# Kernel tuning notes

Measured on AMD Instinct MI355X. Metric: run time of the kernel, lower is better.

The kernel has to match this reference:

```python
import jax, jax.numpy as jnp
import numpy as np
import math

N, M = 512, 31
INP, EMB, ATT = 64, 64, 64
NUM_RELS = 200
SELF_LOOP_IDX = NUM_RELS  # index num_rels is the self-loop relation


def setup_inputs() -> dict:
    key = jax.random.key(0)
    ks = jax.random.split(key, 11)
    s_w = 1.0 / math.sqrt(EMB)
    return {
        "h": jax.random.normal(ks[0], (N, INP), jnp.float32),
        "msg": jax.random.normal(ks[1], (N, M, EMB), jnp.float32),
        "msg_type": jax.random.randint(ks[2], (N, M), 0, NUM_RELS, jnp.int32),
        "r_label_node": jax.random.randint(ks[3], (N,), 0, NUM_RELS, jnp.int32),
        "r_label_msg": jax.random.randint(ks[4], (N, M), 0, NUM_RELS, jnp.int32),
        "W_self": jax.random.normal(ks[5], (INP, EMB), jnp.float32) * s_w,
        "Q": jax.random.normal(ks[6], (NUM_RELS + 1, EMB, ATT), jnp.float32) * s_w,
        "K": jax.random.normal(ks[7], (NUM_RELS + 1, EMB, ATT), jnp.float32) * s_w,
        "V": jax.random.normal(ks[8], (NUM_RELS + 1, EMB, ATT), jnp.float32) * s_w,
        "ffn_w": jax.random.normal(ks[9], (ATT, EMB), jnp.float32) * s_w,
        "ffn_b": jnp.zeros((EMB,), jnp.float32),
    }


def reference(h, msg, msg_type, r_label_node, r_label_msg, W_self, Q, K, V, ffn_w, ffn_b):
    curr = h @ W_self                                        # [N, EMB]
    x = jnp.concatenate([curr[:, None, :], msg], axis=1)     # [N, M+1, EMB]
    qv_idx = jnp.concatenate([r_label_node[:, None], r_label_msg], axis=1)  # [N, M+1]
    self_col = jnp.full((x.shape[0], 1), SELF_LOOP_IDX, msg_type.dtype)
    k_idx = jnp.concatenate([self_col, msg_type], axis=1)    # [N, M+1]
    # relation-indexed per-token projection weights (irregular gather)
    q = jnp.einsum("nme,nmea->nma", x, Q[qv_idx])            # [N, M+1, ATT]
    k = jnp.einsum("nme,nmea->nma", x, K[k_idx])             # [N, M+1, ATT]
    v = jnp.einsum("nme,nmea->nma", x, V[qv_idx])            # [N, M+1, ATT]
    scores = jnp.einsum("nqa,nka->nqk", q, k) / math.sqrt(ATT)
    # NOTE: original code applies softmax over dim=1 (the query axis)
    att = jax.nn.softmax(scores, axis=1)                     # [N, M+1, M+1]
    pooled = jnp.einsum("nqk,nka->nqa", att, v)[:, 0]        # [N, ATT]
    return pooled @ ffn_w + ffn_b                            # [N, EMB]
```

## Files before the change

### kernel.cpp

```cpp
#include <hip/hip_runtime.h>
#include <math.h>

#define NN 512
#define MM 31
#define TT 32
#define EE 64
#define NREL 200
#define NMAT 201
#define SELF_LOOP 200
#define QCAP 192
#define NT 6
#define WSTR 72
#define CPAD 32

typedef short  short8 __attribute__((ext_vector_type(8)));
typedef float  f32x4  __attribute__((ext_vector_type(4)));

__device__ __forceinline__ unsigned short f2bf(float f) {
    union { float f; unsigned int u; } a; a.f = f;
    unsigned int r = a.u + 0x7FFFu + ((a.u >> 16) & 1u);
    return (unsigned short)(r >> 16);
}
__device__ __forceinline__ float bf2f(unsigned short u) {
    union { unsigned int u; float f; } a; a.u = ((unsigned int)u) << 16;
    return a.f;
}

__global__ __launch_bounds__(256) void prep_convert_kernel(
    const float* __restrict__ h, const float* __restrict__ W_self,
    const float* __restrict__ Q, const float* __restrict__ K,
    const float* __restrict__ V,
    const int* __restrict__ msg_type, const int* __restrict__ r_label_node,
    const int* __restrict__ r_label_msg, const float* __restrict__ msg,
    int* __restrict__ cnt_q, int* __restrict__ cnt_k,
    int* __restrict__ list_q, int* __restrict__ list_k,
    unsigned short* __restrict__ wt_q, unsigned short* __restrict__ wt_k,
    unsigned short* __restrict__ wt_v,
    unsigned short* __restrict__ msg_bf, unsigned short* __restrict__ curr_bf,
    unsigned short* __restrict__ k_bf)
{
    const int bid = blockIdx.x, tid = threadIdx.x;

    if (bid < 3 * NMAT) {
        const int r   = bid % NMAT;
        const int mat = bid / NMAT;
        const float* src = (mat == 0 ? Q : mat == 1 ? K : V) + (size_t)r * EE * EE;
        unsigned short* dst = (mat == 0 ? wt_q : mat == 1 ? wt_k : wt_v)
                              + (size_t)r * EE * EE;
        __shared__ unsigned short t_s[EE * WSTR];
        {
            const int e = tid >> 2, aseg = (tid & 3) * 16;
            const float4* s4 = (const float4*)(src + e * EE + aseg);
            float4 f0 = s4[0], f1 = s4[1], f2 = s4[2], f3 = s4[3];
            unsigned short b[16] = {
                f2bf(f0.x), f2bf(f0.y), f2bf(f0.z), f2bf(f0.w),
                f2bf(f1.x), f2bf(f1.y), f2bf(f1.z), f2bf(f1.w),
                f2bf(f2.x), f2bf(f2.y), f2bf(f2.z), f2bf(f2.w),
                f2bf(f3.x), f2bf(f3.y), f2bf(f3.z), f2bf(f3.w) };
            unsigned short* d = &t_s[e * WSTR + aseg];
            *(short8*)d = *(short8*)&b[0];
            *(short8*)(d + 8) = *(short8*)&b[8];
        }
        __syncthreads();
        {
            const int a = tid >> 2, eseg = (tid & 3) * 16;
            unsigned short o[16];
#pragma unroll
            for (int j = 0; j < 16; ++j)
                o[j] = t_s[(eseg + j) * WSTR + a];
            unsigned short* d = dst + a * EE + eseg;
            *(short8*)d = *(short8*)&o[0];
            *(short8*)(d + 8) = *(short8*)&o[8];
        }
        return;
    }

    const int n = bid - 3 * NMAT;

    if (tid < MM) {
        int j  = n * MM + tid;
        int rl = r_label_msg[j];
        int p  = atomicAdd(&cnt_q[rl * CPAD], 1);
        if (p < QCAP) list_q[rl * QCAP + p] = n * TT + tid + 1;
        int mt = msg_type[j];
        int p2 = atomicAdd(&cnt_k[mt * CPAD], 1);
        if (p2 < QCAP) list_k[mt * QCAP + p2] = n * TT + tid + 1;
    } else if (tid == 63) {
        int r = r_label_node[n];
        int p = atomicAdd(&cnt_q[r * CPAD], 1);
        if (p < QCAP) list_q[r * QCAP + p] = n * TT;
    }

    if (tid < MM * EE / 8) {
        const float4* s4 = (const float4*)(msg + (size_t)n * MM * EE) + tid * 2;
        float4 f0 = s4[0], f1 = s4[1];
        unsigned short b[8] = { f2bf(f0.x), f2bf(f0.y), f2bf(f0.z), f2bf(f0.w),
                                f2bf(f1.x), f2bf(f1.y), f2bf(f1.z), f2bf(f1.w) };
        *(short8*)(msg_bf + (size_t)n * MM * EE + tid * 8) = *(short8*)b;
    }

    __shared__ float c_s[EE];
    if (tid < EE) {
        const float* hrow = h + n * EE;
        float acc = 0.f;
#pragma unroll 8
        for (int e = 0; e < EE; ++e)
            acc = fmaf(hrow[e], W_self[e * EE + tid], acc);
        curr_bf[n * EE + tid] = f2bf(acc);
        c_s[tid] = acc;
    }
    __syncthreads();
    if (tid < EE) {
        const float* K200 = K + (size_t)SELF_LOOP * EE * EE;
        float k0 = 0.f;
#pragma unroll 8
        for (int e = 0; e < EE; ++e)
            k0 = fmaf(c_s[e], K200[e * EE + tid], k0);
        k_bf[(size_t)n * TT * EE + tid] = f2bf(k0);
    }
}

__global__ __launch_bounds__(256) void proj_tile_kernel(
    const unsigned short* __restrict__ curr_bf,
    const unsigned short* __restrict__ msg_bf,
    const unsigned short* __restrict__ wt_q,
    const unsigned short* __restrict__ wt_k,
    const unsigned short* __restrict__ wt_v,
    const int* __restrict__ cnt_q, const int* __restrict__ cnt_k,
    const int* __restrict__ list_q, const int* __restrict__ list_k,
    unsigned short* __restrict__ q_bf, unsigned short* __restrict__ k_bf,
    unsigned short* __restrict__ v_bf)
{
    const int r    = blockIdx.x / NT;
    const int tile = blockIdx.x % NT;
    const int tid  = threadIdx.x;
    const int lane = tid & 63;
    const int wave = tid >> 6;
    const int col  = lane & 15;
    const int quad = lane >> 4;

    const int nq = min(cnt_q[r * CPAD], QCAP);
    const int nk = min(cnt_k[r * CPAD], QCAP);
    const int q0 = tile * 32;
    const bool do_q = q0 < nq;
    const bool do_k = q0 < nk;
    if (!do_q && !do_k) return;

    const size_t wbase = (size_t)r * EE * EE;

    if (do_q) {
        const int mtile = wave & 1;
        const unsigned short* wmat = ((wave >> 1) ? wt_v : wt_q) + wbase;
        unsigned short* outp = (wave >> 1) ? v_bf : q_bf;
        const int arow = q0 + mtile * 16 + col;
        int atok = (arow < nq) ? list_q[r * QCAP + arow] : 0;
        {
            int an = atok >> 5, at = atok & 31;
            const unsigned short* aptr = at
                ? (msg_bf + ((size_t)an * MM + (at - 1)) * EE)
                : (curr_bf + (size_t)an * EE);
            f32x4 acc[4] = {{0,0,0,0},{0,0,0,0},{0,0,0,0},{0,0,0,0}};
#pragma unroll
            for (int kk = 0; kk < 2; ++kk) {
                short8 af = *(const short8*)(aptr + kk * 32 + quad * 8);
#pragma unroll
                for (int nt = 0; nt < 4; ++nt) {
                    short8 bf = *(const short8*)(wmat + (nt * 16 + col) * EE + kk * 32 + quad * 8);
                    acc[nt] = __builtin_amdgcn_mfma_f32_16x16x32_bf16(af, bf, acc[nt], 0, 0, 0);
                }
            }
#pragma unroll
            for (int reg = 0; reg < 4; ++reg) {
                int rrow = q0 + mtile * 16 + quad * 4 + reg;
                if (rrow < nq) {
                    int token = list_q[r * QCAP + rrow];
#pragma unroll
                    for (int nt = 0; nt < 4; ++nt)
                        outp[(size_t)token * EE + nt * 16 + col] = f2bf(acc[nt][reg]);
                }
            }
        }
    }

    if (do_k) {
        const int mtile = wave & 1;
        const int nh = wave >> 1;
        const int arow = q0 + mtile * 16 + col;
        int atok = (arow < nk) ? list_k[r * QCAP + arow] : 0;
        int an = atok >> 5, at = atok & 31;
        const unsigned short* aptr = at
            ? (msg_bf + ((size_t)an * MM + (at - 1)) * EE)
            : (curr_bf + (size_t)an * EE);
        const unsigned short* wmat = wt_k + wbase;
        f32x4 acc[2] = {{0,0,0,0},{0,0,0,0}};
#pragma unroll
        for (int kk = 0; kk < 2; ++kk) {
            short8 af = *(const short8*)(aptr + kk * 32 + quad * 8);
#pragma unroll
            for (int j = 0; j < 2; ++j) {
                int nt = nh * 2 + j;
                short8 bf = *(const short8*)(wmat + (nt * 16 + col) * EE + kk * 32 + quad * 8);
                acc[j] = __builtin_amdgcn_mfma_f32_16x16x32_bf16(af, bf, acc[j], 0, 0, 0);
            }
        }
#pragma unroll
        for (int reg = 0; reg < 4; ++reg) {
            int rrow = q0 + mtile * 16 + quad * 4 + reg;
            if (rrow < nk) {
                int token = list_k[r * QCAP + rrow];
#pragma unroll
                for (int j = 0; j < 2; ++j)
                    k_bf[(size_t)token * EE + (nh * 2 + j) * 16 + col] = f2bf(acc[j][reg]);
            }
        }
    }
}

__global__ __launch_bounds__(256) void attn_kernel(
    const unsigned short* __restrict__ q_bf,
    const unsigned short* __restrict__ k_bf,
    const unsigned short* __restrict__ v_bf,
    const float* __restrict__ ffn_w, const float* __restrict__ ffn_b,
    float* __restrict__ out)
{
    const int n = blockIdx.x, tid = threadIdx.x;
    const int lane = tid & 63, wave = tid >> 6;
    const int col = lane & 15, quad = lane >> 4;
    __shared__ float s_s[TT][TT + 1];
    __shared__ float att0[TT];
    __shared__ float pooled[EE];

    {
        const int mi = wave & 1, ni = wave >> 1;
        const unsigned short* qrow = q_bf + ((size_t)n * TT + mi * 16 + col) * EE;
        const unsigned short* krow = k_bf + ((size_t)n * TT + ni * 16 + col) * EE;
        f32x4 acc = {0, 0, 0, 0};
#pragma unroll
        for (int kk = 0; kk < 2; ++kk) {
            short8 a = *(const short8*)(qrow + kk * 32 + quad * 8);
            short8 b = *(const short8*)(krow + kk * 32 + quad * 8);
            acc = __builtin_amdgcn_mfma_f32_16x16x32_bf16(a, b, acc, 0, 0, 0);
        }
#pragma unroll
        for (int reg = 0; reg < 4; ++reg)
            s_s[mi * 16 + quad * 4 + reg][ni * 16 + col] = acc[reg] * 0.125f;
    }
    __syncthreads();

    if (tid < TT) {
        float mx = -INFINITY;
#pragma unroll
        for (int qi = 0; qi < TT; ++qi) mx = fmaxf(mx, s_s[qi][tid]);
        float sum = 0.f;
#pragma unroll
        for (int qi = 0; qi < TT; ++qi) sum += __expf(s_s[qi][tid] - mx);
        att0[tid] = __expf(s_s[0][tid] - mx) / sum;
    }
    __syncthreads();

    if (tid < EE) {
        const unsigned short* vp = v_bf + (size_t)n * TT * EE + tid;
        float acc = 0.f;
#pragma unroll 8
        for (int ki = 0; ki < TT; ++ki)
            acc = fmaf(att0[ki], bf2f(vp[ki * EE]), acc);
        pooled[tid] = acc;
    }
    __syncthreads();

    if (tid < EE) {
        float acc = ffn_b[tid];
#pragma unroll 8
        for (int a = 0; a < EE; ++a)
            acc = fmaf(pooled[a], ffn_w[a * EE + tid], acc);
        out[n * EE + tid] = acc;
    }
}

extern "C" void kernel_launch(void* const* d_in, const int* in_sizes, int n_in,
                              void* d_out, int out_size, void* d_ws, size_t ws_size,
                              hipStream_t stream) {
    const float* h            = (const float*)d_in[0];
    const float* msg          = (const float*)d_in[1];
    const int*   msg_type     = (const int*)  d_in[2];
    const int*   r_label_node = (const int*)  d_in[3];
    const int*   r_label_msg  = (const int*)  d_in[4];
    const float* W_self       = (const float*)d_in[5];
    const float* Q            = (const float*)d_in[6];
    const float* K            = (const float*)d_in[7];
    const float* V            = (const float*)d_in[8];
    const float* ffn_w        = (const float*)d_in[9];
    const float* ffn_b        = (const float*)d_in[10];
    float*       out          = (float*)d_out;

    int* cnt_q  = (int*)d_ws;
    int* cnt_k  = cnt_q + NREL * CPAD;
    int* list_q = cnt_k + NREL * CPAD;
    int* list_k = list_q + NREL * QCAP;
    unsigned short* wt_q = (unsigned short*)(list_k + NREL * QCAP);
    unsigned short* wt_k = wt_q + (size_t)NMAT * EE * EE;
    unsigned short* wt_v = wt_k + (size_t)NMAT * EE * EE;
    unsigned short* msg_bf  = wt_v + (size_t)NMAT * EE * EE;
    unsigned short* curr_bf = msg_bf + (size_t)NN * MM * EE;
    unsigned short* q_bf = curr_bf + NN * EE;
    unsigned short* k_bf = q_bf + (size_t)NN * TT * EE;
    unsigned short* v_bf = k_bf + (size_t)NN * TT * EE;

    hipMemsetAsync(cnt_q, 0, 2 * NREL * CPAD * sizeof(int), stream);
    prep_convert_kernel<<<3 * NMAT + NN, 256, 0, stream>>>(
        h, W_self, Q, K, V, msg_type, r_label_node, r_label_msg, msg,
        cnt_q, cnt_k, list_q, list_k, wt_q, wt_k, wt_v,
        msg_bf, curr_bf, k_bf);
    proj_tile_kernel<<<NREL * NT, 256, 0, stream>>>(
        curr_bf, msg_bf, wt_q, wt_k, wt_v, cnt_q, cnt_k, list_q, list_k,
        q_bf, k_bf, v_bf);
    attn_kernel<<<NN, 256, 0, stream>>>(q_bf, k_bf, v_bf, ffn_w, ffn_b, out);
}
```

Baseline: 111.3 us.

## Fuse three kernels into one persistent kernel with grid barriers

Merges the prep, projection and attention kernels into a single persistent kernel of 512 blocks that loop over tasks, separated by software grid-wide barriers built on atomics. This removes two kernel launch gaps and tail effects between stages. It also splits the per-node 64x64 matvecs across all four waves with shared-memory partial sums. In exchange it adds spin barriers that rely on all 512 blocks being co-resident, and a spin timeout that could silently break correctness if they are not.

```diff
diff --git a/kernel.cpp b/kernel.cpp
--- a/kernel.cpp
+++ b/kernel.cpp
@@ -12,6 +12,7 @@
 #define NT 6
 #define WSTR 72
 #define CPAD 32
+#define GRID 512
 
 typedef short  short8 __attribute__((ext_vector_type(8)));
 typedef float  f32x4  __attribute__((ext_vector_type(4)));
@@ -26,135 +27,160 @@
     return a.f;
 }
 
-__global__ __launch_bounds__(256) void prep_convert_kernel(
+__device__ __forceinline__ void grid_barrier(int* bar) {
+    __threadfence();
+    __syncthreads();
+    if (threadIdx.x == 0) {
+        __hip_atomic_fetch_add(bar, 1, __ATOMIC_ACQ_REL, __HIP_MEMORY_SCOPE_AGENT);
+        long spins = 0;
+        while (__hip_atomic_load(bar, __ATOMIC_ACQUIRE, __HIP_MEMORY_SCOPE_AGENT) < GRID) {
+            if (++spins > (1L << 22)) break;
+            __builtin_amdgcn_s_sleep(1);
+        }
+    }
+    __syncthreads();
+    __threadfence();
+}
+
+__global__ __launch_bounds__(256, 4) void fused_kernel(
     const float* __restrict__ h, const float* __restrict__ W_self,
     const float* __restrict__ Q, const float* __restrict__ K,
     const float* __restrict__ V,
     const int* __restrict__ msg_type, const int* __restrict__ r_label_node,
     const int* __restrict__ r_label_msg, const float* __restrict__ msg,
+    const float* __restrict__ ffn_w, const float* __restrict__ ffn_b,
     int* __restrict__ cnt_q, int* __restrict__ cnt_k,
+    int* __restrict__ bars,
     int* __restrict__ list_q, int* __restrict__ list_k,
     unsigned short* __restrict__ wt_q, unsigned short* __restrict__ wt_k,
     unsigned short* __restrict__ wt_v,
     unsigned short* __restrict__ msg_bf, unsigned short* __restrict__ curr_bf,
-    unsigned short* __restrict__ k_bf)
+    unsigned short* __restrict__ q_bf, unsigned short* __restrict__ k_bf,
+    unsigned short* __restrict__ v_bf,
+    float* __restrict__ out)
 {
     const int bid = blockIdx.x, tid = threadIdx.x;
-
-    if (bid < 3 * NMAT) {
-        const int r   = bid % NMAT;
-        const int mat = bid / NMAT;
-        const float* src = (mat == 0 ? Q : mat == 1 ? K : V) + (size_t)r * EE * EE;
-        unsigned short* dst = (mat == 0 ? wt_q : mat == 1 ? wt_k : wt_v)
-                              + (size_t)r * EE * EE;
-        __shared__ unsigned short t_s[EE * WSTR];
-        {
-            const int e = tid >> 2, aseg = (tid & 3) * 16;
-            const float4* s4 = (const float4*)(src + e * EE + aseg);
-            float4 f0 = s4[0], f1 = s4[1], f2 = s4[2], f3 = s4[3];
-            unsigned short b[16] = {
-                f2bf(f0.x), f2bf(f0.y), f2bf(f0.z), f2bf(f0.w),
-                f2bf(f1.x), f2bf(f1.y), f2bf(f1.z), f2bf(f1.w),
-                f2bf(f2.x), f2bf(f2.y), f2bf(f2.z), f2bf(f2.w),
-                f2bf(f3.x), f2bf(f3.y), f2bf(f3.z), f2bf(f3.w) };
-            unsigned short* d = &t_s[e * WSTR + aseg];
-            *(short8*)d = *(short8*)&b[0];
-            *(short8*)(d + 8) = *(short8*)&b[8];
-        }
-        __syncthreads();
-        {
-            const int a = tid >> 2, eseg = (tid & 3) * 16;
-            unsigned short o[16];
-#pragma unroll
-            for (int j = 0; j < 16; ++j)
-                o[j] = t_s[(eseg + j) * WSTR + a];
-            unsigned short* d = dst + a * EE + eseg;
-            *(short8*)d = *(short8*)&o[0];
-            *(short8*)(d + 8) = *(short8*)&o[8];
-        }
-        return;
+    const int lane = tid & 63, wave = tid >> 6;
+    const int col = lane & 15, quad = lane >> 4;
+
+    __shared__ union SM {
+        unsigned short t_s[EE * WSTR];
+        struct { float part[4][EE]; float c_s[EE]; } np;
+        struct { float s_s[TT][TT + 1]; float att0[TT]; float pooled[EE]; } at;
+    } sm;
+
+    for (int task = bid; task < 3 * NMAT + NN; task += GRID) {
+        if (task < 3 * NMAT) {
+            const int r   = task % NMAT;
+            const int mat = task / NMAT;
+            const float* src = (mat == 0 ? Q : mat == 1 ? K : V) + (size_t)r * EE * EE;
+            unsigned short* dst = (mat == 0 ? wt_q : mat == 1 ? wt_k : wt_v)
+                                  + (size_t)r * EE * EE;
+            {
+                const int e = tid >> 2, aseg = (tid & 3) * 16;
+                const float4* s4 = (const float4*)(src + e * EE + aseg);
+                float4 f0 = s4[0], f1 = s4[1], f2 = s4[2], f3 = s4[3];
+                unsigned short b[16] = {
+                    f2bf(f0.x), f2bf(f0.y), f2bf(f0.z), f2bf(f0.w),
+                    f2bf(f1.x), f2bf(f1.y), f2bf(f1.z), f2bf(f1.w),
+                    f2bf(f2.x), f2bf(f2.y), f2bf(f2.z), f2bf(f2.w),
+                    f2bf(f3.x), f2bf(f3.y), f2bf(f3.z), f2bf(f3.w) };
+                unsigned short* d = &sm.t_s[e * WSTR + aseg];
+                *(short8*)d = *(short8*)&b[0];
+                *(short8*)(d + 8) = *(short8*)&b[8];
+            }
+            __syncthreads();
+            {
+                const int a = tid >> 2, eseg = (tid & 3) * 16;
+                unsigned short o[16];
+#pragma unroll
+                for (int j = 0; j < 16; ++j)
+                    o[j] = sm.t_s[(eseg + j) * WSTR + a];
+                unsigned short* d = dst + a * EE + eseg;
+                *(short8*)d = *(short8*)&o[0];
+                *(short8*)(d + 8) = *(short8*)&o[8];
+            }
+            __syncthreads();
+        } else {
+            const int n = task - 3 * NMAT;
+
+            if (tid < MM) {
+                int j  = n * MM + tid;
+                int rl = r_label_msg[j];
+                int p  = atomicAdd(&cnt_q[rl * CPAD], 1);
+                if (p < QCAP) list_q[rl * QCAP + p] = n * TT + tid + 1;
+                int mt = msg_type[j];
+                int p2 = atomicAdd(&cnt_k[mt * CPAD], 1);
+                if (p2 < QCAP) list_k[mt * QCAP + p2] = n * TT + tid + 1;
+            } else if (tid == 63) {
+                int r = r_label_node[n];
+                int p = atomicAdd(&cnt_q[r * CPAD], 1);
+                if (p < QCAP) list_q[r * QCAP + p] = n * TT;
+            }
+
+            if (tid < MM * EE / 8) {
+                const float4* s4 = (const float4*)(msg + (size_t)n * MM * EE) + tid * 2;
+                float4 f0 = s4[0], f1 = s4[1];
+                unsigned short b[8] = { f2bf(f0.x), f2bf(f0.y), f2bf(f0.z), f2bf(f0.w),
+                                        f2bf(f1.x), f2bf(f1.y), f2bf(f1.z), f2bf(f1.w) };
+                *(short8*)(msg_bf + (size_t)n * MM * EE + tid * 8) = *(short8*)b;
+            }
+
+            const int c = tid & 63, part = tid >> 6;
+            {
+                const float* hrow = h + n * EE;
+                float acc = 0.f;
+#pragma unroll
+                for (int e = 0; e < 16; ++e)
+                    acc = fmaf(hrow[part * 16 + e], W_self[(part * 16 + e) * EE + c], acc);
+                sm.np.part[part][c] = acc;
+            }
+            __syncthreads();
+            if (tid < EE) {
+                float cv = sm.np.part[0][tid] + sm.np.part[1][tid]
+                         + sm.np.part[2][tid] + sm.np.part[3][tid];
+                curr_bf[n * EE + tid] = f2bf(cv);
+                sm.np.c_s[tid] = cv;
+            }
+            __syncthreads();
+            {
+                const float* K200 = K + (size_t)SELF_LOOP * EE * EE;
+                float acc = 0.f;
+#pragma unroll
+                for (int e = 0; e < 16; ++e)
+                    acc = fmaf(sm.np.c_s[part * 16 + e], K200[(part * 16 + e) * EE + c], acc);
+                sm.np.part[part][c] = acc;
+            }
+            __syncthreads();
+            if (tid < EE) {
+                float k0 = sm.np.part[0][tid] + sm.np.part[1][tid]
+                         + sm.np.part[2][tid] + sm.np.part[3][tid];
+                k_bf[(size_t)n * TT * EE + tid] = f2bf(k0);
+            }
+            __syncthreads();
+        }
     }
-
-    const int n = bid - 3 * NMAT;
-
-    if (tid < MM) {
-        int j  = n * MM + tid;
-        int rl = r_label_msg[j];
-        int p  = atomicAdd(&cnt_q[rl * CPAD], 1);
-        if (p < QCAP) list_q[rl * QCAP + p] = n * TT + tid + 1;
-        int mt = msg_type[j];
-        int p2 = atomicAdd(&cnt_k[mt * CPAD], 1);
-        if (p2 < QCAP) list_k[mt * QCAP + p2] = n * TT + tid + 1;
-    } else if (tid == 63) {
-        int r = r_label_node[n];
-        int p = atomicAdd(&cnt_q[r * CPAD], 1);
-        if (p < QCAP) list_q[r * QCAP + p] = n * TT;
-    }
-
-    if (tid < MM * EE / 8) {
-        const float4* s4 = (const float4*)(msg + (size_t)n * MM * EE) + tid * 2;
-        float4 f0 = s4[0], f1 = s4[1];
-        unsigned short b[8] = { f2bf(f0.x), f2bf(f0.y), f2bf(f0.z), f2bf(f0.w),
-                                f2bf(f1.x), f2bf(f1.y), f2bf(f1.z), f2bf(f1.w) };
-        *(short8*)(msg_bf + (size_t)n * MM * EE + tid * 8) = *(short8*)b;
-    }
-
-    __shared__ float c_s[EE];
-    if (tid < EE) {
-        const float* hrow = h + n * EE;
-        float acc = 0.f;
-#pragma unroll 8
-        for (int e = 0; e < EE; ++e)
-            acc = fmaf(hrow[e], W_self[e * EE + tid], acc);
-        curr_bf[n * EE + tid] = f2bf(acc);
-        c_s[tid] = acc;
-    }
-    __syncthreads();
-    if (tid < EE) {
-        const float* K200 = K + (size_t)SELF_LOOP * EE * EE;
-        float k0 = 0.f;
-#pragma unroll 8
-        for (int e = 0; e < EE; ++e)
-            k0 = fmaf(c_s[e], K200[e * EE + tid], k0);
-        k_bf[(size_t)n * TT * EE + tid] = f2bf(k0);
-    }
-}
-
-__global__ __launch_bounds__(256) void proj_tile_kernel(
-    const unsigned short* __restrict__ curr_bf,
-    const unsigned short* __restrict__ msg_bf,
-    const unsigned short* __restrict__ wt_q,
-    const unsigned short* __restrict__ wt_k,
-    const unsigned short* __restrict__ wt_v,
-    const int* __restrict__ cnt_q, const int* __restrict__ cnt_k,
-    const int* __restrict__ list_q, const int* __restrict__ list_k,
-    unsigned short* __restrict__ q_bf, unsigned short* __restrict__ k_bf,
-    unsigned short* __restrict__ v_bf)
-{
-    const int r    = blockIdx.x / NT;
-    const int tile = blockIdx.x % NT;
-    const int tid  = threadIdx.x;
-    const int lane = tid & 63;
-    const int wave = tid >> 6;
-    const int col  = lane & 15;
-    const int quad = lane >> 4;
-
-    const int nq = min(cnt_q[r * CPAD], QCAP);
-    const int nk = min(cnt_k[r * CPAD], QCAP);
-    const int q0 = tile * 32;
-    const bool do_q = q0 < nq;
-    const bool do_k = q0 < nk;
-    if (!do_q && !do_k) return;
-
-    const size_t wbase = (size_t)r * EE * EE;
-
-    if (do_q) {
-        const int mtile = wave & 1;
-        const unsigned short* wmat = ((wave >> 1) ? wt_v : wt_q) + wbase;
-        unsigned short* outp = (wave >> 1) ? v_bf : q_bf;
-        const int arow = q0 + mtile * 16 + col;
-        int atok = (arow < nq) ? list_q[r * QCAP + arow] : 0;
-        {
+    grid_barrier(&bars[0]);
+
+    for (int task = bid; task < NREL * NT; task += GRID) {
+        const int r    = task / NT;
+        const int tile = task % NT;
+
+        const int nq = min(cnt_q[r * CPAD], QCAP);
+        const int nk = min(cnt_k[r * CPAD], QCAP);
+        const int q0 = tile * 32;
+        const bool do_q = q0 < nq;
+        const bool do_k = q0 < nk;
+        if (!do_q && !do_k) continue;
+
+        const size_t wbase = (size_t)r * EE * EE;
+
+        if (do_q) {
+            const int mtile = wave & 1;
+            const unsigned short* wmat = ((wave >> 1) ? wt_v : wt_q) + wbase;
+            unsigned short* outp = (wave >> 1) ? v_bf : q_bf;
+            const int arow = q0 + mtile * 16 + col;
+            int atok = (arow < nq) ? list_q[r * QCAP + arow] : 0;
             int an = atok >> 5, at = atok & 31;
             const unsigned short* aptr = at
                 ? (msg_bf + ((size_t)an * MM + (at - 1)) * EE)
@@ -180,100 +206,91 @@
                 }
             }
         }
+
+        if (do_k) {
+            const int mtile = wave & 1;
+            const int nh = wave >> 1;
+            const int arow = q0 + mtile * 16 + col;
+            int atok = (arow < nk) ? list_k[r * QCAP + arow] : 0;
+            int an = atok >> 5, at = atok & 31;
+            const unsigned short* aptr = at
+                ? (msg_bf + ((size_t)an * MM + (at - 1)) * EE)
+                : (curr_bf + (size_t)an * EE);
+            const unsigned short* wmat = wt_k + wbase;
+            f32x4 acc[2] = {{0,0,0,0},{0,0,0,0}};
+#pragma unroll
+            for (int kk = 0; kk < 2; ++kk) {
+                short8 af = *(const short8*)(aptr + kk * 32 + quad * 8);
+#pragma unroll
+                for (int j = 0; j < 2; ++j) {
+                    int nt = nh * 2 + j;
+                    short8 bf = *(const short8*)(wmat + (nt * 16 + col) * EE + kk * 32 + quad * 8);
+                    acc[j] = __builtin_amdgcn_mfma_f32_16x16x32_bf16(af, bf, acc[j], 0, 0, 0);
+                }
+            }
+#pragma unroll
+            for (int reg = 0; reg < 4; ++reg) {
+                int rrow = q0 + mtile * 16 + quad * 4 + reg;
+                if (rrow < nk) {
+                    int token = list_k[r * QCAP + rrow];
+#pragma unroll
+                    for (int j = 0; j < 2; ++j)
+                        k_bf[(size_t)token * EE + (nh * 2 + j) * 16 + col] = f2bf(acc[j][reg]);
+                }
+            }
+        }
     }
-
-    if (do_k) {
-        const int mtile = wave & 1;
-        const int nh = wave >> 1;
-        const int arow = q0 + mtile * 16 + col;
-        int atok = (arow < nk) ? list_k[r * QCAP + arow] : 0;
-        int an = atok >> 5, at = atok & 31;
-        const unsigned short* aptr = at
-            ? (msg_bf + ((size_t)an * MM + (at - 1)) * EE)
-            : (curr_bf + (size_t)an * EE);
-        const unsigned short* wmat = wt_k + wbase;
-        f32x4 acc[2] = {{0,0,0,0},{0,0,0,0}};
-#pragma unroll
-        for (int kk = 0; kk < 2; ++kk) {
-            short8 af = *(const short8*)(aptr + kk * 32 + quad * 8);
-#pragma unroll
-            for (int j = 0; j < 2; ++j) {
-                int nt = nh * 2 + j;
-                short8 bf = *(const short8*)(wmat + (nt * 16 + col) * EE + kk * 32 + quad * 8);
-                acc[j] = __builtin_amdgcn_mfma_f32_16x16x32_bf16(af, bf, acc[j], 0, 0, 0);
-            }
-        }
-#pragma unroll
-        for (int reg = 0; reg < 4; ++reg) {
-            int rrow = q0 + mtile * 16 + quad * 4 + reg;
-            if (rrow < nk) {
-                int token = list_k[r * QCAP + rrow];
-#pragma unroll
-                for (int j = 0; j < 2; ++j)
-                    k_bf[(size_t)token * EE + (nh * 2 + j) * 16 + col] = f2bf(acc[j][reg]);
-            }
-        }
-    }
-}
-
-__global__ __launch_bounds__(256) void attn_kernel(
-    const unsigned short* __restrict__ q_bf,
-    const unsigned short* __restrict__ k_bf,
-    const unsigned short* __restrict__ v_bf,
-    const float* __restrict__ ffn_w, const float* __restrict__ ffn_b,
-    float* __restrict__ out)
-{
-    const int n = blockIdx.x, tid = threadIdx.x;
-    const int lane = tid & 63, wave = tid >> 6;
-    const int col = lane & 15, quad = lane >> 4;
-    __shared__ float s_s[TT][TT + 1];
-    __shared__ float att0[TT];
-    __shared__ float pooled[EE];
-
-    {
-        const int mi = wave & 1, ni = wave >> 1;
-        const unsigned short* qrow = q_bf + ((size_t)n * TT + mi * 16 + col) * EE;
-        const unsigned short* krow = k_bf + ((size_t)n * TT + ni * 16 + col) * EE;
-        f32x4 acc = {0, 0, 0, 0};
-#pragma unroll
-        for (int kk = 0; kk < 2; ++kk) {
-            short8 a = *(const short8*)(qrow + kk * 32 + quad * 8);
-            short8 b = *(const short8*)(krow + kk * 32 + quad * 8);
-            acc = __builtin_amdgcn_mfma_f32_16x16x32_bf16(a, b, acc, 0, 0, 0);
-        }
-#pragma unroll
-        for (int reg = 0; reg < 4; ++reg)
-            s_s[mi * 16 + quad * 4 + reg][ni * 16 + col] = acc[reg] * 0.125f;
-    }
-    __syncthreads();
-
-    if (tid < TT) {
-        float mx = -INFINITY;
-#pragma unroll
-        for (int qi = 0; qi < TT; ++qi) mx = fmaxf(mx, s_s[qi][tid]);
-        float sum = 0.f;
-#pragma unroll
-        for (int qi = 0; qi < TT; ++qi) sum += __expf(s_s[qi][tid] - mx);
-        att0[tid] = __expf(s_s[0][tid] - mx) / sum;
-    }
-    __syncthreads();
-
-    if (tid < EE) {
-        const unsigned short* vp = v_bf + (size_t)n * TT * EE + tid;
-        float acc = 0.f;
+    grid_barrier(&bars[32]);
+
+    for (int task = bid; task < NN; task += GRID) {
+        const int n = task;
+
+        {
+            const int mi = wave & 1, ni = wave >> 1;
+            const unsigned short* qrow = q_bf + ((size_t)n * TT + mi * 16 + col) * EE;
+            const unsigned short* krow = k_bf + ((size_t)n * TT + ni * 16 + col) * EE;
+            f32x4 acc = {0, 0, 0, 0};
+#pragma unroll
+            for (int kk = 0; kk < 2; ++kk) {
+                short8 a = *(const short8*)(qrow + kk * 32 + quad * 8);
+                short8 b = *(const short8*)(krow + kk * 32 + quad * 8);
+                acc = __builtin_amdgcn_mfma_f32_16x16x32_bf16(a, b, acc, 0, 0, 0);
+            }
+#pragma unroll
+            for (int reg = 0; reg < 4; ++reg)
+                sm.at.s_s[mi * 16 + quad * 4 + reg][ni * 16 + col] = acc[reg] * 0.125f;
+        }
+        __syncthreads();
+
+        if (tid < TT) {
+            float mx = -INFINITY;
+#pragma unroll
+            for (int qi = 0; qi < TT; ++qi) mx = fmaxf(mx, sm.at.s_s[qi][tid]);
+            float sum = 0.f;
+#pragma unroll
+            for (int qi = 0; qi < TT; ++qi) sum += __expf(sm.at.s_s[qi][tid] - mx);
+            sm.at.att0[tid] = __expf(sm.at.s_s[0][tid] - mx) / sum;
+        }
+        __syncthreads();
+
+        if (tid < EE) {
+            const unsigned short* vp = v_bf + (size_t)n * TT * EE + tid;
+            float acc = 0.f;
 #pragma unroll 8
-        for (int ki = 0; ki < TT; ++ki)
-            acc = fmaf(att0[ki], bf2f(vp[ki * EE]), acc);
-        pooled[tid] = acc;
-    }
-    __syncthreads();
-
-    if (tid < EE) {
-        float acc = ffn_b[tid];
+            for (int ki = 0; ki < TT; ++ki)
+                acc = fmaf(sm.at.att0[ki], bf2f(vp[ki * EE]), acc);
+            sm.at.pooled[tid] = acc;
+        }
+        __syncthreads();
+
+        if (tid < EE) {
+            float acc = ffn_b[tid];
 #pragma unroll 8
-        for (int a = 0; a < EE; ++a)
-            acc = fmaf(pooled[a], ffn_w[a * EE + tid], acc);
-        out[n * EE + tid] = acc;
+            for (int a = 0; a < EE; ++a)
+                acc = fmaf(sm.at.pooled[a], ffn_w[a * EE + tid], acc);
+            out[n * EE + tid] = acc;
+        }
+        __syncthreads();
     }
 }
 
@@ -295,7 +312,8 @@
 
     int* cnt_q  = (int*)d_ws;
     int* cnt_k  = cnt_q + NREL * CPAD;
-    int* list_q = cnt_k + NREL * CPAD;
+    int* bars   = cnt_k + NREL * CPAD;
+    int* list_q = bars + 64;
     int* list_k = list_q + NREL * QCAP;
     unsigned short* wt_q = (unsigned short*)(list_k + NREL * QCAP);
     unsigned short* wt_k = wt_q + (size_t)NMAT * EE * EE;
@@ -306,13 +324,10 @@
     unsigned short* k_bf = q_bf + (size_t)NN * TT * EE;
     unsigned short* v_bf = k_bf + (size_t)NN * TT * EE;
 
-    hipMemsetAsync(cnt_q, 0, 2 * NREL * CPAD * sizeof(int), stream);
-    prep_convert_kernel<<<3 * NMAT + NN, 256, 0, stream>>>(
+    hipMemsetAsync(cnt_q, 0, (2 * NREL * CPAD + 64) * sizeof(int), stream);
+    fused_kernel<<<GRID, 256, 0, stream>>>(
         h, W_self, Q, K, V, msg_type, r_label_node, r_label_msg, msg,
-        cnt_q, cnt_k, list_q, list_k, wt_q, wt_k, wt_v,
-        msg_bf, curr_bf, k_bf);
-    proj_tile_kernel<<<NREL * NT, 256, 0, stream>>>(
-        curr_bf, msg_bf, wt_q, wt_k, wt_v, cnt_q, cnt_k, list_q, list_k,
-        q_bf, k_bf, v_bf);
-    attn_kernel<<<NN, 256, 0, stream>>>(q_bf, k_bf, v_bf, ffn_w, ffn_b, out);
-}
+        ffn_w, ffn_b,
+        cnt_q, cnt_k, bars, list_q, list_k, wt_q, wt_k, wt_v,
+        msg_bf, curr_bf, q_bf, k_bf, v_bf, out);
+}
```

After: 352.7 us. +216.9%, slower.

## Fuse per-node projection and attention into one kernel, drop relation bucketing

Applied to the files above, without the earlier changes.

Replaces the bucket-by-relation MFMA projection pipeline (memset, atomic list building, tiled projection kernel, separate attention kernel) with one per-node kernel. The weight transpose/bf16 conversion stays as its own kernel. The per-node kernel loads msg and computes curr into shared memory, then does per-token scalar dot products against the gathered bf16 Q/K/V rows, and finishes with attention, softmax, pooling and FFN in place. This removes the memset, the atomics, two launches and the global round-trips of q/k/v, at the cost of scalar FMA projections and uncoalesced per-token weight gathers instead of MFMA.

```diff
diff --git a/kernel.cpp b/kernel.cpp
--- a/kernel.cpp
+++ b/kernel.cpp
@@ -8,13 +8,9 @@
 #define NREL 200
 #define NMAT 201
 #define SELF_LOOP 200
-#define QCAP 192
-#define NT 6
 #define WSTR 72
-#define CPAD 32
 
 typedef short  short8 __attribute__((ext_vector_type(8)));
-typedef float  f32x4  __attribute__((ext_vector_type(4)));
 
 __device__ __forceinline__ unsigned short f2bf(float f) {
     union { float f; unsigned int u; } a; a.f = f;
@@ -26,251 +22,156 @@
     return a.f;
 }
 
-__global__ __launch_bounds__(256) void prep_convert_kernel(
-    const float* __restrict__ h, const float* __restrict__ W_self,
+__global__ __launch_bounds__(256) void convert_kernel(
     const float* __restrict__ Q, const float* __restrict__ K,
     const float* __restrict__ V,
-    const int* __restrict__ msg_type, const int* __restrict__ r_label_node,
-    const int* __restrict__ r_label_msg, const float* __restrict__ msg,
-    int* __restrict__ cnt_q, int* __restrict__ cnt_k,
-    int* __restrict__ list_q, int* __restrict__ list_k,
     unsigned short* __restrict__ wt_q, unsigned short* __restrict__ wt_k,
-    unsigned short* __restrict__ wt_v,
-    unsigned short* __restrict__ msg_bf, unsigned short* __restrict__ curr_bf,
-    unsigned short* __restrict__ k_bf)
+    unsigned short* __restrict__ wt_v)
 {
     const int bid = blockIdx.x, tid = threadIdx.x;
-
-    if (bid < 3 * NMAT) {
-        const int r   = bid % NMAT;
-        const int mat = bid / NMAT;
-        const float* src = (mat == 0 ? Q : mat == 1 ? K : V) + (size_t)r * EE * EE;
-        unsigned short* dst = (mat == 0 ? wt_q : mat == 1 ? wt_k : wt_v)
-                              + (size_t)r * EE * EE;
-        __shared__ unsigned short t_s[EE * WSTR];
-        {
-            const int e = tid >> 2, aseg = (tid & 3) * 16;
-            const float4* s4 = (const float4*)(src + e * EE + aseg);
-            float4 f0 = s4[0], f1 = s4[1], f2 = s4[2], f3 = s4[3];
-            unsigned short b[16] = {
-                f2bf(f0.x), f2bf(f0.y), f2bf(f0.z), f2bf(f0.w),
-                f2bf(f1.x), f2bf(f1.y), f2bf(f1.z), f2bf(f1.w),
-                f2bf(f2.x), f2bf(f2.y), f2bf(f2.z), f2bf(f2.w),
-                f2bf(f3.x), f2bf(f3.y), f2bf(f3.z), f2bf(f3.w) };
-            unsigned short* d = &t_s[e * WSTR + aseg];
-            *(short8*)d = *(short8*)&b[0];
-            *(short8*)(d + 8) = *(short8*)&b[8];
-        }
-        __syncthreads();
-        {
-            const int a = tid >> 2, eseg = (tid & 3) * 16;
-            unsigned short o[16];
-#pragma unroll
-            for (int j = 0; j < 16; ++j)
-                o[j] = t_s[(eseg + j) * WSTR + a];
-            unsigned short* d = dst + a * EE + eseg;
-            *(short8*)d = *(short8*)&o[0];
-            *(short8*)(d + 8) = *(short8*)&o[8];
-        }
-        return;
-    }
-
-    const int n = bid - 3 * NMAT;
-
-    if (tid < MM) {
-        int j  = n * MM + tid;
-        int rl = r_label_msg[j];
-        int p  = atomicAdd(&cnt_q[rl * CPAD], 1);
-        if (p < QCAP) list_q[rl * QCAP + p] = n * TT + tid + 1;
-        int mt = msg_type[j];
-        int p2 = atomicAdd(&cnt_k[mt * CPAD], 1);
-        if (p2 < QCAP) list_k[mt * QCAP + p2] = n * TT + tid + 1;
-    } else if (tid == 63) {
-        int r = r_label_node[n];
-        int p = atomicAdd(&cnt_q[r * CPAD], 1);
-        if (p < QCAP) list_q[r * QCAP + p] = n * TT;
-    }
-
-    if (tid < MM * EE / 8) {
-        const float4* s4 = (const float4*)(msg + (size_t)n * MM * EE) + tid * 2;
-        float4 f0 = s4[0], f1 = s4[1];
-        unsigned short b[8] = { f2bf(f0.x), f2bf(f0.y), f2bf(f0.z), f2bf(f0.w),
-                                f2bf(f1.x), f2bf(f1.y), f2bf(f1.z), f2bf(f1.w) };
-        *(short8*)(msg_bf + (size_t)n * MM * EE + tid * 8) = *(short8*)b;
-    }
-
-    __shared__ float c_s[EE];
-    if (tid < EE) {
-        const float* hrow = h + n * EE;
-        float acc = 0.f;
-#pragma unroll 8
-        for (int e = 0; e < EE; ++e)
-            acc = fmaf(hrow[e], W_self[e * EE + tid], acc);
-        curr_bf[n * EE + tid] = f2bf(acc);
-        c_s[tid] = acc;
-    }
-    __syncthreads();
-    if (tid < EE) {
-        const float* K200 = K + (size_t)SELF_LOOP * EE * EE;
-        float k0 = 0.f;
-#pragma unroll 8
-        for (int e = 0; e < EE; ++e)
-            k0 = fmaf(c_s[e], K200[e * EE + tid], k0);
-        k_bf[(size_t)n * TT * EE + tid] = f2bf(k0);
-    }
-}
-
-__global__ __launch_bounds__(256) void proj_tile_kernel(
-    const unsigned short* __restrict__ curr_bf,
-    const unsigned short* __restrict__ msg_bf,
+    const int r   = bid % NMAT;
+    const int mat = bid / NMAT;
+    const float* src = (mat == 0 ? Q : mat == 1 ? K : V) + (size_t)r * EE * EE;
+    unsigned short* dst = (mat == 0 ? wt_q : mat == 1 ? wt_k : wt_v)
+                          + (size_t)r * EE * EE;
+    __shared__ unsigned short t_s[EE * WSTR];
+    {
+        const int e = tid >> 2, aseg = (tid & 3) * 16;
+        const float4* s4 = (const float4*)(src + e * EE + aseg);
+        float4 f0 = s4[0], f1 = s4[1], f2 = s4[2], f3 = s4[3];
+        unsigned short b[16] = {
+            f2bf(f0.x), f2bf(f0.y), f2bf(f0.z), f2bf(f0.w),
+            f2bf(f1.x), f2bf(f1.y), f2bf(f1.z), f2bf(f1.w),
+            f2bf(f2.x), f2bf(f2.y), f2bf(f2.z), f2bf(f2.w),
+            f2bf(f3.x), f2bf(f3.y), f2bf(f3.z), f2bf(f3.w) };
+        unsigned short* d = &t_s[e * WSTR + aseg];
+        *(short8*)d = *(short8*)&b[0];
+        *(short8*)(d + 8) = *(short8*)&b[8];
+    }
+    __syncthreads();
+    {
+        const int a = tid >> 2, eseg = (tid & 3) * 16;
+        unsigned short o[16];
+#pragma unroll
+        for (int j = 0; j < 16; ++j)
+            o[j] = t_s[(eseg + j) * WSTR + a];
+        unsigned short* d = dst + a * EE + eseg;
+        *(short8*)d = *(short8*)&o[0];
+        *(short8*)(d + 8) = *(short8*)&o[8];
+    }
+}
+
+__global__ __launch_bounds__(256) void node_kernel(
+    const float* __restrict__ h, const float* __restrict__ W_self,
+    const float* __restrict__ msg,
+    const int* __restrict__ msg_type, const int* __restrict__ r_label_node,
+    const int* __restrict__ r_label_msg,
     const unsigned short* __restrict__ wt_q,
     const unsigned short* __restrict__ wt_k,
     const unsigned short* __restrict__ wt_v,
-    const int* __restrict__ cnt_q, const int* __restrict__ cnt_k,
-    const int* __restrict__ list_q, const int* __restrict__ list_k,
-    unsigned short* __restrict__ q_bf, unsigned short* __restrict__ k_bf,
-    unsigned short* __restrict__ v_bf)
-{
-    const int r    = blockIdx.x / NT;
-    const int tile = blockIdx.x % NT;
-    const int tid  = threadIdx.x;
-    const int lane = tid & 63;
-    const int wave = tid >> 6;
-    const int col  = lane & 15;
-    const int quad = lane >> 4;
-
-    const int nq = min(cnt_q[r * CPAD], QCAP);
-    const int nk = min(cnt_k[r * CPAD], QCAP);
-    const int q0 = tile * 32;
-    const bool do_q = q0 < nq;
-    const bool do_k = q0 < nk;
-    if (!do_q && !do_k) return;
-
-    const size_t wbase = (size_t)r * EE * EE;
-
-    if (do_q) {
-        const int mtile = wave & 1;
-        const unsigned short* wmat = ((wave >> 1) ? wt_v : wt_q) + wbase;
-        unsigned short* outp = (wave >> 1) ? v_bf : q_bf;
-        const int arow = q0 + mtile * 16 + col;
-        int atok = (arow < nq) ? list_q[r * QCAP + arow] : 0;
-        {
-            int an = atok >> 5, at = atok & 31;
-            const unsigned short* aptr = at
-                ? (msg_bf + ((size_t)an * MM + (at - 1)) * EE)
-                : (curr_bf + (size_t)an * EE);
-            f32x4 acc[4] = {{0,0,0,0},{0,0,0,0},{0,0,0,0},{0,0,0,0}};
-#pragma unroll
-            for (int kk = 0; kk < 2; ++kk) {
-                short8 af = *(const short8*)(aptr + kk * 32 + quad * 8);
-#pragma unroll
-                for (int nt = 0; nt < 4; ++nt) {
-                    short8 bf = *(const short8*)(wmat + (nt * 16 + col) * EE + kk * 32 + quad * 8);
-                    acc[nt] = __builtin_amdgcn_mfma_f32_16x16x32_bf16(af, bf, acc[nt], 0, 0, 0);
-                }
-            }
-#pragma unroll
-            for (int reg = 0; reg < 4; ++reg) {
-                int rrow = q0 + mtile * 16 + quad * 4 + reg;
-                if (rrow < nq) {
-                    int token = list_q[r * QCAP + rrow];
-#pragma unroll
-                    for (int nt = 0; nt < 4; ++nt)
-                        outp[(size_t)token * EE + nt * 16 + col] = f2bf(acc[nt][reg]);
-                }
-            }
-        }
-    }
-
-    if (do_k) {
-        const int mtile = wave & 1;
-        const int nh = wave >> 1;
-        const int arow = q0 + mtile * 16 + col;
-        int atok = (arow < nk) ? list_k[r * QCAP + arow] : 0;
-        int an = atok >> 5, at = atok & 31;
-        const unsigned short* aptr = at
-            ? (msg_bf + ((size_t)an * MM + (at - 1)) * EE)
-            : (curr_bf + (size_t)an * EE);
-        const unsigned short* wmat = wt_k + wbase;
-        f32x4 acc[2] = {{0,0,0,0},{0,0,0,0}};
-#pragma unroll
-        for (int kk = 0; kk < 2; ++kk) {
-            short8 af = *(const short8*)(aptr + kk * 32 + quad * 8);
-#pragma unroll
-            for (int j = 0; j < 2; ++j) {
-                int nt = nh * 2 + j;
-                short8 bf = *(const short8*)(wmat + (nt * 16 + col) * EE + kk * 32 + quad * 8);
-                acc[j] = __builtin_amdgcn_mfma_f32_16x16x32_bf16(af, bf, acc[j], 0, 0, 0);
-            }
-        }
-#pragma unroll
-        for (int reg = 0; reg < 4; ++reg) {
-            int rrow = q0 + mtile * 16 + quad * 4 + reg;
-            if (rrow < nk) {
-                int token = list_k[r * QCAP + rrow];
-#pragma unroll
-                for (int j = 0; j < 2; ++j)
-                    k_bf[(size_t)token * EE + (nh * 2 + j) * 16 + col] = f2bf(acc[j][reg]);
-            }
-        }
-    }
-}
-
-__global__ __launch_bounds__(256) void attn_kernel(
-    const unsigned short* __restrict__ q_bf,
-    const unsigned short* __restrict__ k_bf,
-    const unsigned short* __restrict__ v_bf,
     const float* __restrict__ ffn_w, const float* __restrict__ ffn_b,
     float* __restrict__ out)
 {
     const int n = blockIdx.x, tid = threadIdx.x;
-    const int lane = tid & 63, wave = tid >> 6;
-    const int col = lane & 15, quad = lane >> 4;
+
+    __shared__ float x_s[TT][EE + 4];
+    __shared__ float q_s[TT][EE + 4], k_s[TT][EE + 4], v_s[TT][EE + 4];
     __shared__ float s_s[TT][TT + 1];
-    __shared__ float att0[TT];
-    __shared__ float pooled[EE];
-
-    {
-        const int mi = wave & 1, ni = wave >> 1;
-        const unsigned short* qrow = q_bf + ((size_t)n * TT + mi * 16 + col) * EE;
-        const unsigned short* krow = k_bf + ((size_t)n * TT + ni * 16 + col) * EE;
-        f32x4 acc = {0, 0, 0, 0};
-#pragma unroll
-        for (int kk = 0; kk < 2; ++kk) {
-            short8 a = *(const short8*)(qrow + kk * 32 + quad * 8);
-            short8 b = *(const short8*)(krow + kk * 32 + quad * 8);
-            acc = __builtin_amdgcn_mfma_f32_16x16x32_bf16(a, b, acc, 0, 0, 0);
+    __shared__ float att0[TT], pooled[EE];
+    __shared__ float part[4][EE];
+    __shared__ int qv_s[TT], kk_s[TT];
+
+    if (tid < MM * EE / 8) {
+        const float4* s4 = (const float4*)(msg + (size_t)n * MM * EE) + tid * 2;
+        float4 f0 = s4[0], f1 = s4[1];
+        const int idx = tid * 8, m = idx >> 6, e = idx & 63;
+        float* d = &x_s[m + 1][e];
+        *(float4*)d = f0; *(float4*)(d + 4) = f1;
+    }
+    if (tid < MM) {
+        qv_s[tid + 1] = r_label_msg[n * MM + tid];
+        kk_s[tid + 1] = msg_type[n * MM + tid];
+    } else if (tid == 40) {
+        qv_s[0] = r_label_node[n];
+        kk_s[0] = SELF_LOOP;
+    }
+    {
+        const int c = tid & 63, p4 = tid >> 6;
+        const float* hrow = h + n * EE;
+        float acc = 0.f;
+#pragma unroll
+        for (int e = 0; e < 16; ++e)
+            acc = fmaf(hrow[p4 * 16 + e], W_self[(p4 * 16 + e) * EE + c], acc);
+        part[p4][c] = acc;
+    }
+    __syncthreads();
+    if (tid < EE)
+        x_s[0][tid] = part[0][tid] + part[1][tid] + part[2][tid] + part[3][tid];
+    __syncthreads();
+
+    {
+        const int a = tid & 63;
+        const int wv = tid >> 6;
+        for (int iter = 0; iter < 8; ++iter) {
+            const int t = iter * 4 + wv;
+            const int rq = qv_s[t], rk = kk_s[t];
+            const unsigned short* Wq = wt_q + ((size_t)rq << 12) + a * EE;
+            const unsigned short* Wv = wt_v + ((size_t)rq << 12) + a * EE;
+            const unsigned short* Wk = wt_k + ((size_t)rk << 12) + a * EE;
+            const float* xr = &x_s[t][0];
+            float aq = 0.f, ak = 0.f, av = 0.f;
+#pragma unroll
+            for (int e8 = 0; e8 < 8; ++e8) {
+                short8 wq8 = *(const short8*)(Wq + e8 * 8);
+                short8 wk8 = *(const short8*)(Wk + e8 * 8);
+                short8 wv8 = *(const short8*)(Wv + e8 * 8);
+#pragma unroll
+                for (int j = 0; j < 8; ++j) {
+                    float xv = xr[e8 * 8 + j];
+                    aq = fmaf(xv, bf2f(((unsigned short*)&wq8)[j]), aq);
+                    ak = fmaf(xv, bf2f(((unsigned short*)&wk8)[j]), ak);
+                    av = fmaf(xv, bf2f(((unsigned short*)&wv8)[j]), av);
+                }
+            }
+            q_s[t][a] = aq; k_s[t][a] = ak; v_s[t][a] = av;
         }
-#pragma unroll
-        for (int reg = 0; reg < 4; ++reg)
-            s_s[mi * 16 + quad * 4 + reg][ni * 16 + col] = acc[reg] * 0.125f;
+    }
+    __syncthreads();
+
+    {
+        const int ki = tid & 31;
+        for (int qi = tid >> 5; qi < TT; qi += 8) {
+            const float4* qp = (const float4*)&q_s[qi][0];
+            const float4* kp = (const float4*)&k_s[ki][0];
+            float acc = 0.f;
+            for (int e4 = 0; e4 < EE / 4; ++e4) {
+                float4 a = qp[e4], b = kp[e4];
+                acc += a.x * b.x + a.y * b.y + a.z * b.z + a.w * b.w;
+            }
+            s_s[qi][ki] = acc * 0.125f;
+        }
     }
     __syncthreads();
 
     if (tid < TT) {
         float mx = -INFINITY;
-#pragma unroll
         for (int qi = 0; qi < TT; ++qi) mx = fmaxf(mx, s_s[qi][tid]);
         float sum = 0.f;
-#pragma unroll
         for (int qi = 0; qi < TT; ++qi) sum += __expf(s_s[qi][tid] - mx);
         att0[tid] = __expf(s_s[0][tid] - mx) / sum;
     }
     __syncthreads();
 
     if (tid < EE) {
-        const unsigned short* vp = v_bf + (size_t)n * TT * EE + tid;
         float acc = 0.f;
-#pragma unroll 8
         for (int ki = 0; ki < TT; ++ki)
-            acc = fmaf(att0[ki], bf2f(vp[ki * EE]), acc);
+            acc = fmaf(att0[ki], v_s[ki][tid], acc);
         pooled[tid] = acc;
     }
     __syncthreads();
 
     if (tid < EE) {
         float acc = ffn_b[tid];
-#pragma unroll 8
         for (int a = 0; a < EE; ++a)
             acc = fmaf(pooled[a], ffn_w[a * EE + tid], acc);
         out[n * EE + tid] = acc;
@@ -293,26 +194,12 @@
     const float* ffn_b        = (const float*)d_in[10];
     float*       out          = (float*)d_out;
 
-    int* cnt_q  = (int*)d_ws;
-    int* cnt_k  = cnt_q + NREL * CPAD;
-    int* list_q = cnt_k + NREL * CPAD;
-    int* list_k = list_q + NREL * QCAP;
-    unsigned short* wt_q = (unsigned short*)(list_k + NREL * QCAP);
+    unsigned short* wt_q = (unsigned short*)d_ws;
     unsigned short* wt_k = wt_q + (size_t)NMAT * EE * EE;
     unsigned short* wt_v = wt_k + (size_t)NMAT * EE * EE;
-    unsigned short* msg_bf  = wt_v + (size_t)NMAT * EE * EE;
-    unsigned short* curr_bf = msg_bf + (size_t)NN * MM * EE;
-    unsigned short* q_bf = curr_bf + NN * EE;
-    unsigned short* k_bf = q_bf + (size_t)NN * TT * EE;
-    unsigned short* v_bf = k_bf + (size_t)NN * TT * EE;
-
-    hipMemsetAsync(cnt_q, 0, 2 * NREL * CPAD * sizeof(int), stream);
-    prep_convert_kernel<<<3 * NMAT + NN, 256, 0, stream>>>(
-        h, W_self, Q, K, V, msg_type, r_label_node, r_label_msg, msg,
-        cnt_q, cnt_k, list_q, list_k, wt_q, wt_k, wt_v,
-        msg_bf, curr_bf, k_bf);
-    proj_tile_kernel<<<NREL * NT, 256, 0, stream>>>(
-        curr_bf, msg_bf, wt_q, wt_k, wt_v, cnt_q, cnt_k, list_q, list_k,
-        q_bf, k_bf, v_bf);
-    attn_kernel<<<NN, 256, 0, stream>>>(q_bf, k_bf, v_bf, ffn_w, ffn_b, out);
-}
+
+    convert_kernel<<<3 * NMAT, 256, 0, stream>>>(Q, K, V, wt_q, wt_k, wt_v);
+    node_kernel<<<NN, 256, 0, stream>>>(
+        h, W_self, msg, msg_type, r_label_node, r_label_msg,
+        wt_q, wt_k, wt_v, ffn_w, ffn_b, out);
+}
```

New measurement: 183.6 us. 65.0% more time.
